# Kernel optimization log

Measured on AMD Instinct MI355X. Metric: run time of the kernel, lower is better.

Reference implementation:

```python
import jax, jax.numpy as jnp
import numpy as np

B, S, T, D, H, HD = 1, 2048, 256, 3072, 24, 128
FF = 4 * D
EPS_LN = 1e-6
EPS_RMS = 1e-6


def _layernorm(x):
    m = jnp.mean(x, axis=-1, keepdims=True)
    v = jnp.mean(jnp.square(x - m), axis=-1, keepdims=True)
    return (x - m) * jax.lax.rsqrt(v + EPS_LN)


def _rmsnorm(x, w):
    return x * jax.lax.rsqrt(jnp.mean(jnp.square(x), axis=-1, keepdims=True) + EPS_RMS) * w


def _rope_interleaved(x, cos, sin):
    # x: [B,S,H,HD], cos/sin: [S,HD//2]; non-neox (interleaved) style
    x1 = x[..., 0::2]
    x2 = x[..., 1::2]
    c = cos[None, :, None, :]
    s = sin[None, :, None, :]
    o1 = x1 * c - x2 * s
    o2 = x2 * c + x1 * s
    return jnp.stack([o1, o2], axis=-1).reshape(x.shape)


def setup_inputs() -> dict:
    key = jax.random.key(0)
    ks = jax.random.split(key, 12)

    def n(k, shape, scale):
        return jax.random.normal(k, shape, dtype=jnp.float32) * scale

    # real RoPE tables
    pos = np.arange(S, dtype=np.float64)
    inv_freq = 1.0 / (10000.0 ** (np.arange(0, HD, 2, dtype=np.float64) / HD))
    ang = np.outer(pos, inv_freq)  # [S, HD//2]

    return {
        "img": n(ks[0], (B, S, D), 1.0),
        "vec": n(ks[1], (B, D), 1.0),
        "cos": jnp.asarray(np.cos(ang), jnp.float32),
        "sin": jnp.asarray(np.sin(ang), jnp.float32),
        "k_txt": n(ks[2], (B, T, H, HD), 1.0),
        "v_txt": n(ks[3], (B, T, H, HD), 1.0),
        "mod_w": n(ks[4], (D, 6 * D), 0.02),
        "mod_b": jnp.zeros((6 * D,), jnp.float32),
        "qkv_w": n(ks[5], (D, 3 * D), 0.02),
        "qkv_b": jnp.zeros((3 * D,), jnp.float32),
        "qn_w": jnp.ones((HD,), jnp.float32),
        "kn_w": jnp.ones((HD,), jnp.float32),
        "proj_w": n(ks[6], (D, D), 0.02),
        "proj_b": jnp.zeros((D,), jnp.float32),
        "mlp_w1": n(ks[7], (D, FF), 0.02),
        "mlp_b1": jnp.zeros((FF,), jnp.float32),
        "mlp_w2": n(ks[8], (FF, D), 0.02),
        "mlp_b2": jnp.zeros((D,), jnp.float32),
    }


def reference(img, vec, cos, sin, k_txt, v_txt, mod_w, mod_b, qkv_w, qkv_b,
              qn_w, kn_w, proj_w, proj_b, mlp_w1, mlp_b1, mlp_w2, mlp_b2):
    # modulation: silu(vec) -> linear -> 6 chunks, each [B,1,D]
    mod = jax.nn.silu(vec) @ mod_w + mod_b
    (a_shift, a_scale, a_gate, m_shift, m_scale, m_gate) = [
        m[:, None, :] for m in jnp.split(mod, 6, axis=-1)
    ]

    # LayerNorm (no affine) + scale/shift modulate
    x = _layernorm(img) * (1.0 + a_scale) + a_shift

    qkv = (x @ qkv_w + qkv_b).reshape(B, S, 3, H, HD)
    q, k, v = qkv[:, :, 0], qkv[:, :, 1], qkv[:, :, 2]
    q = _rmsnorm(q, qn_w)
    k = _rmsnorm(k, kn_w)
    q = _rope_interleaved(q, cos, sin)
    k = _rope_interleaved(k, cos, sin)

    # concat text KV cache (no RoPE on text tokens)
    k_all = jnp.concatenate([k, k_txt], axis=1)  # [B,S+T,H,HD]
    v_all = jnp.concatenate([v, v_txt], axis=1)

    scale = 1.0 / jnp.sqrt(jnp.asarray(HD, jnp.float32))
    scores = jnp.einsum('bqhd,bkhd->bhqk', q, k_all) * scale
    probs = jax.nn.softmax(scores, axis=-1)
    attn = jnp.einsum('bhqk,bkhd->bqhd', probs, v_all).reshape(B, S, D)

    attn_out = attn @ proj_w + proj_b

    # ScaleResidualLayerNormScaleShift
    residual = img + a_gate * attn_out
    mlp_in = _layernorm(residual) * (1.0 + m_scale) + m_shift

    mlp_out = jax.nn.gelu(mlp_in @ mlp_w1 + mlp_b1, approximate=True) @ mlp_w2 + mlp_b2
    return residual + m_gate * mlp_out
```

## Files before the change

### kernel.cpp

```cpp
#include <hip/hip_runtime.h>

typedef short short8 __attribute__((ext_vector_type(8)));
typedef float f32x4 __attribute__((ext_vector_type(4)));

#define DEV static __device__ __forceinline__

DEV unsigned short f2bf(float f) {
  union { float f; unsigned u; } v; v.f = f;
  unsigned u = v.u;
  unsigned r = u + 0x7fffu + ((u >> 16) & 1u);
  return (unsigned short)(r >> 16);
}
DEV float bf2f(unsigned short b) {
  union { unsigned u; float f; } v; v.u = ((unsigned)b) << 16;
  return v.f;
}
DEV void load_lds16(const void* g, void* l) {
  __builtin_amdgcn_global_load_lds(
      (const __attribute__((address_space(1))) unsigned int*)g,
      (__attribute__((address_space(3))) unsigned int*)l, 16, 0, 0);
}
DEV int swz(int L) { return L ^ ((L >> 3) & 0x30); }

__global__ __launch_bounds__(256) void zero_mod(const float* __restrict__ b, float* __restrict__ out) {
  int j = blockIdx.x * 256 + threadIdx.x;
  out[j] = b[j];
}

__global__ __launch_bounds__(256) void mod_gemv(const float* __restrict__ vec,
                                                const float* __restrict__ W,
                                                float* __restrict__ out) {
  __shared__ float sv[192];
  int tid = threadIdx.x;
  int kb = blockIdx.y * 192;
  if (tid < 192) {
    float x = vec[kb + tid];
    sv[tid] = x / (1.f + __expf(-x));
  }
  __syncthreads();
  int j = blockIdx.x * 256 + tid;
  float a0 = 0, a1 = 0, a2 = 0, a3 = 0;
  for (int i = 0; i < 192; i += 4) {
    a0 += sv[i + 0] * W[(size_t)(kb + i + 0) * 18432 + j];
    a1 += sv[i + 1] * W[(size_t)(kb + i + 1) * 18432 + j];
    a2 += sv[i + 2] * W[(size_t)(kb + i + 2) * 18432 + j];
    a3 += sv[i + 3] * W[(size_t)(kb + i + 3) * 18432 + j];
  }
  atomicAdd(&out[j], a0 + a1 + a2 + a3);
}

__global__ __launch_bounds__(256) void ln_kernel(const float* __restrict__ in,
                                                 const float* __restrict__ mod,
                                                 int shift_off, int scale_off,
                                                 unsigned short* __restrict__ out) {
  int rowb = blockIdx.x;
  const float* x = in + (size_t)rowb * 3072;
  int tid = threadIdx.x;
  float s = 0.f, ss = 0.f;
  float4 v[3];
#pragma unroll
  for (int r = 0; r < 3; r++) {
    v[r] = *(const float4*)&x[r * 1024 + tid * 4];
    s += v[r].x + v[r].y + v[r].z + v[r].w;
    ss += v[r].x * v[r].x + v[r].y * v[r].y + v[r].z * v[r].z + v[r].w * v[r].w;
  }
#pragma unroll
  for (int m = 32; m; m >>= 1) { s += __shfl_xor(s, m); ss += __shfl_xor(ss, m); }
  __shared__ float red[8];
  int w = tid >> 6, lane = tid & 63;
  if (lane == 0) { red[w] = s; red[4 + w] = ss; }
  __syncthreads();
  s = red[0] + red[1] + red[2] + red[3];
  ss = red[4] + red[5] + red[6] + red[7];
  float mean = s * (1.f / 3072.f);
  float var = ss * (1.f / 3072.f) - mean * mean;
  float rstd = rsqrtf(var + 1e-6f);
#pragma unroll
  for (int r = 0; r < 3; r++) {
    int c = r * 1024 + tid * 4;
    float xv[4] = {v[r].x, v[r].y, v[r].z, v[r].w};
#pragma unroll
    for (int i = 0; i < 4; i++) {
      float o = (xv[i] - mean) * rstd * (1.f + mod[scale_off + c + i]) + mod[shift_off + c + i];
      out[(size_t)rowb * 3072 + c + i] = f2bf(o);
    }
  }
}

__global__ __launch_bounds__(256) void transpose_k(const float* __restrict__ src,
                                                   unsigned short* __restrict__ dst,
                                                   int K, int N) {
  __shared__ float t[64][65];
  int n0 = blockIdx.x * 64, k0 = blockIdx.y * 64;
  int tid = threadIdx.x;
#pragma unroll
  for (int i = 0; i < 16; i++) {
    int lin = i * 256 + tid;
    int r = lin >> 6, c = lin & 63;
    t[r][c] = src[(size_t)(k0 + r) * N + n0 + c];
  }
  __syncthreads();
#pragma unroll
  for (int i = 0; i < 16; i++) {
    int lin = i * 256 + tid;
    int rn = lin >> 6, cn = lin & 63;
    dst[(size_t)(n0 + rn) * K + k0 + cn] = f2bf(t[cn][rn]);
  }
}

__global__ __launch_bounds__(256) void vt_k(const unsigned short* __restrict__ qkvb,
                                            const float* __restrict__ v_txt,
                                            unsigned short* __restrict__ vt) {
  int h = blockIdx.y;
  int c8 = blockIdx.x * 2 + (threadIdx.x >> 7);
  int d = threadIdx.x & 127;
  int kvb = c8 * 8;
  short8 o;
  if (kvb < 2048) {
#pragma unroll
    for (int j = 0; j < 8; j++)
      o[j] = (short)qkvb[(size_t)(kvb + j) * 9216 + 6144 + h * 128 + d];
  } else {
#pragma unroll
    for (int j = 0; j < 8; j++)
      o[j] = (short)f2bf(v_txt[((size_t)(kvb + j - 2048) * 24 + h) * 128 + d]);
  }
  *(short8*)&vt[((size_t)h * 128 + d) * 2304 + kvb] = o;
}

template <int EPI>
__global__ __launch_bounds__(512, 2) void gemm8(const unsigned short* __restrict__ A,
                                                const unsigned short* __restrict__ Bt,
                                                const float* __restrict__ bias,
                                                unsigned short* __restrict__ outb,
                                                int N, int ldk, int klen, size_t zstride) {
  __shared__ unsigned short As[4][8192];
  __shared__ unsigned short Bs[4][8192];
  const int tid = threadIdx.x, lane = tid & 63, w = tid >> 6;
  const int wr = w >> 2, wc = w & 3;
  const int lr = lane & 15, lk = lane >> 4;

  const int bm = blockIdx.y * 256, bn = blockIdx.x * 256;
  const int kbase = blockIdx.z * klen;
  const int NT = klen >> 5;

  const int D0 = tid * 16;
  const int D1 = 8192 + tid * 16;
  const int L0 = swz(D0), L1 = swz(D1);
  const unsigned short* sA0 = A + (size_t)(bm + (L0 >> 6)) * ldk + kbase + ((L0 & 63) >> 1);
  const unsigned short* sA1 = A + (size_t)(bm + (L1 >> 6)) * ldk + kbase + ((L1 & 63) >> 1);
  const unsigned short* sB0 = Bt + (size_t)(bn + (L0 >> 6)) * ldk + kbase + ((L0 & 63) >> 1);
  const unsigned short* sB1 = Bt + (size_t)(bn + (L1 >> 6)) * ldk + kbase + ((L1 & 63) >> 1);

  int aoff[8], boff[4];
#pragma unroll
  for (int mi = 0; mi < 8; mi++)
    aoff[mi] = swz(((wr * 128 + mi * 16 + lr) << 6) | (lk << 4));
#pragma unroll
  for (int ni = 0; ni < 4; ni++)
    boff[ni] = swz(((wc * 64 + ni * 16 + lr) << 6) | (lk << 4));

  f32x4 acc[8][4];
#pragma unroll
  for (int i = 0; i < 8; i++)
#pragma unroll
    for (int j = 0; j < 4; j++) acc[i][j] = (f32x4){0.f, 0.f, 0.f, 0.f};

#pragma unroll
  for (int j = 0; j < 3; j++) {
    load_lds16(sA0 + j * 32, (char*)As + j * 16384 + D0);
    load_lds16(sA1 + j * 32, (char*)As + j * 16384 + D1);
    load_lds16(sB0 + j * 32, (char*)Bs + j * 16384 + D0);
    load_lds16(sB1 + j * 32, (char*)Bs + j * 16384 + D1);
  }
  asm volatile("s_waitcnt vmcnt(8)" ::: "memory");
  __builtin_amdgcn_sched_barrier(0);
  __builtin_amdgcn_s_barrier();

  for (int t = 0; t < NT; ++t) {
    const int rt = t & 3;
    char* Ab = (char*)As + rt * 16384;
    char* Bb = (char*)Bs + rt * 16384;
    const int ss = (t + 3) & 3;
    const int sk = (t + 3) * 32;
    const bool stg = (t + 3) < NT;

    short8 af[8], bf[4];
#pragma unroll
    for (int mi = 0; mi < 8; mi++) af[mi] = *(const short8*)(Ab + aoff[mi]);
#pragma unroll
    for (int ni = 0; ni < 4; ni++) bf[ni] = *(const short8*)(Bb + boff[ni]);
    if (stg) {
      load_lds16(sA0 + sk, (char*)As + ss * 16384 + D0);
      load_lds16(sA1 + sk, (char*)As + ss * 16384 + D1);
      load_lds16(sB0 + sk, (char*)Bs + ss * 16384 + D0);
      load_lds16(sB1 + sk, (char*)Bs + ss * 16384 + D1);
    }
    __builtin_amdgcn_s_setprio(1);
#pragma unroll
    for (int mi = 0; mi < 8; mi++)
#pragma unroll
      for (int ni = 0; ni < 4; ni++)
        acc[mi][ni] = __builtin_amdgcn_mfma_f32_16x16x32_bf16(af[mi], bf[ni], acc[mi][ni], 0, 0, 0);
    __builtin_amdgcn_s_setprio(0);
    if (t < NT - 3) {
      asm volatile("s_waitcnt vmcnt(8)" ::: "memory");
    } else if (t == NT - 3) {
      asm volatile("s_waitcnt vmcnt(4)" ::: "memory");
    } else if (t == NT - 2) {
      asm volatile("s_waitcnt vmcnt(0)" ::: "memory");
    }
    __builtin_amdgcn_sched_barrier(0);
    __builtin_amdgcn_s_barrier();
  }

  const size_t zoff = (size_t)blockIdx.z * zstride;
#pragma unroll
  for (int mi = 0; mi < 8; mi++) {
#pragma unroll
    for (int ni = 0; ni < 4; ni++) {
      int row0 = bm + wr * 128 + mi * 16 + lk * 4;
      int col = bn + wc * 64 + ni * 16 + lr;
#pragma unroll
      for (int r = 0; r < 4; r++) {
        float vv = acc[mi][ni][r];
        if (EPI == 0) {
          outb[(size_t)(row0 + r) * N + col] = f2bf(vv + bias[col]);
        } else if (EPI == 2) {
          float x = vv + bias[col];
          float y = 0.7978845608028654f * (x + 0.044715f * x * x * x);
          float th = 1.f - 2.f / (__expf(2.f * y) + 1.f);
          outb[(size_t)(row0 + r) * N + col] = f2bf(0.5f * x * (1.f + th));
        } else {
          outb[zoff + (size_t)(row0 + r) * N + col] = f2bf(vv);
        }
      }
    }
  }
}

template <int NS>
__global__ __launch_bounds__(256) void sk_epi(const unsigned short* __restrict__ pb,
                                              const float* __restrict__ bias,
                                              const float* __restrict__ addsrc,
                                              const float* __restrict__ gate,
                                              float* __restrict__ out) {
  const int N = 3072;
  const size_t MN = (size_t)2048 * 3072;
  int row = blockIdx.y;
  int col = blockIdx.x * 1024 + threadIdx.x * 4;
  size_t idx = (size_t)row * N + col;
  float4 a = *(const float4*)(addsrc + idx);
  float4 b = *(const float4*)(bias + col);
  float4 g = *(const float4*)(gate + col);
  float sum[4] = {b.x, b.y, b.z, b.w};
#pragma unroll
  for (int s = 0; s < NS; s++) {
    const unsigned short* p = pb + s * MN + idx;
#pragma unroll
    for (int i = 0; i < 4; i++) sum[i] += bf2f(p[i]);
  }
  float4 o;
  o.x = a.x + g.x * sum[0];
  o.y = a.y + g.y * sum[1];
  o.z = a.z + g.z * sum[2];
  o.w = a.w + g.w * sum[3];
  *(float4*)(out + idx) = o;
}

__global__ __launch_bounds__(256) void sk_epiq(const unsigned short* __restrict__ p0,
                                               const unsigned short* __restrict__ p1,
                                               const float* __restrict__ bias,
                                               unsigned short* __restrict__ out) {
  const int N = 9216;
  int row = blockIdx.y;
  int col = blockIdx.x * 1024 + threadIdx.x * 4;
  size_t idx = (size_t)row * N + col;
#pragma unroll
  for (int i = 0; i < 4; i++)
    out[idx + i] = f2bf(bf2f(p0[idx + i]) + bf2f(p1[idx + i]) + bias[col + i]);
}

__global__ __launch_bounds__(64) void qkv_post(const unsigned short* __restrict__ qkv,
                                               const float* __restrict__ k_txt,
                                               const float* __restrict__ cosb,
                                               const float* __restrict__ sinb,
                                               const float* __restrict__ qn,
                                               const float* __restrict__ kn,
                                               unsigned short* __restrict__ qb,
                                               unsigned short* __restrict__ kb) {
  int s = blockIdx.x, h = blockIdx.y;
  int lane = threadIdx.x;
  int d0 = lane * 2;
  if (s < 2048) {
    const unsigned short* rowp = qkv + (size_t)s * 9216;
    float c = cosb[s * 64 + lane], sn = sinb[s * 64 + lane];
    const float ascale = 0.08838834764831845f;
    {
      float a = bf2f(rowp[h * 128 + d0]), b = bf2f(rowp[h * 128 + d0 + 1]);
      float sq = a * a + b * b;
#pragma unroll
      for (int m = 32; m; m >>= 1) sq += __shfl_xor(sq, m);
      float rr = rsqrtf(sq * (1.f / 128.f) + 1e-6f);
      float x1 = a * rr * qn[d0], x2 = b * rr * qn[d0 + 1];
      float o1 = (x1 * c - x2 * sn) * ascale;
      float o2 = (x2 * c + x1 * sn) * ascale;
      size_t off = ((size_t)h * 2048 + s) * 128 + d0;
      qb[off] = f2bf(o1); qb[off + 1] = f2bf(o2);
    }
    {
      float a = bf2f(rowp[3072 + h * 128 + d0]), b = bf2f(rowp[3072 + h * 128 + d0 + 1]);
      float sq = a * a + b * b;
#pragma unroll
      for (int m = 32; m; m >>= 1) sq += __shfl_xor(sq, m);
      float rr = rsqrtf(sq * (1.f / 128.f) + 1e-6f);
      float x1 = a * rr * kn[d0], x2 = b * rr * kn[d0 + 1];
      float o1 = x1 * c - x2 * sn;
      float o2 = x2 * c + x1 * sn;
      size_t off = ((size_t)h * 2304 + s) * 128 + d0;
      kb[off] = f2bf(o1); kb[off + 1] = f2bf(o2);
    }
  } else {
    int t = s - 2048;
    size_t src = ((size_t)t * 24 + h) * 128 + d0;
    size_t off = ((size_t)h * 2304 + s) * 128 + d0;
    kb[off] = f2bf(k_txt[src]); kb[off + 1] = f2bf(k_txt[src + 1]);
  }
}

__global__ __launch_bounds__(512) void attn_k(const unsigned short* __restrict__ qb,
                                              const unsigned short* __restrict__ kb,
                                              const unsigned short* __restrict__ vt,
                                              unsigned short* __restrict__ out) {
  __shared__ unsigned short Ks[3][8192];
  __shared__ unsigned short Vs[3][8192];
  __shared__ unsigned short Ps[8][32 * 72];
  int h = blockIdx.y, q0 = blockIdx.x * 256;
  int tid = threadIdx.x, lane = tid & 63, w = tid >> 6;
  int lr = lane & 15, lk = lane >> 4;

  const unsigned short* kh = kb + (size_t)h * 2304 * 128;
  const unsigned short* vth = vt + (size_t)h * 128 * 2304;

  short8 qf[2][4];
#pragma unroll
  for (int mi = 0; mi < 2; mi++)
#pragma unroll
    for (int kf = 0; kf < 4; kf++)
      qf[mi][kf] = *(const short8*)&qb[((size_t)h * 2048 + q0 + w * 32 + mi * 16 + lr) * 128 + kf * 32 + lk * 8];

  const int kR0 = (tid * 16) >> 8, kR1 = (tid * 16 + 8192) >> 8;
  const int kCc = ((tid * 16) >> 4) & 15;
  const int kOf0 = kR0 * 128 + ((kCc ^ (kR0 & 15)) * 8);
  const int kOf1 = kR1 * 128 + ((kCc ^ (kR1 & 15)) * 8);
  const int vR0 = (tid * 16) >> 7, vR1 = (tid * 16 + 8192) >> 7;
  const int vCc = ((tid * 16) >> 4) & 7;
  const int vOf0 = vR0 * 2304 + ((vCc ^ (vR0 & 7)) * 8);
  const int vOf1 = vR1 * 2304 + ((vCc ^ (vR1 & 7)) * 8);

  float mrow[2][4], lsum[2][4];
#pragma unroll
  for (int mi = 0; mi < 2; mi++)
#pragma unroll
    for (int r = 0; r < 4; r++) { mrow[mi][r] = -1e30f; lsum[mi][r] = 0.f; }
  f32x4 oacc[2][8];
#pragma unroll
  for (int mi = 0; mi < 2; mi++)
#pragma unroll
    for (int i = 0; i < 8; i++) oacc[mi][i] = (f32x4){0.f, 0.f, 0.f, 0.f};

#pragma unroll
  for (int j = 0; j < 2; j++) {
    int kv = j * 64;
    load_lds16(kh + (size_t)kv * 128 + kOf0, (char*)Ks[j] + tid * 16);
    load_lds16(kh + (size_t)kv * 128 + kOf1, (char*)Ks[j] + tid * 16 + 8192);
    load_lds16(vth + kv + vOf0, (char*)Vs[j] + tid * 16);
    load_lds16(vth + kv + vOf1, (char*)Vs[j] + tid * 16 + 8192);
  }
  asm volatile("s_waitcnt vmcnt(4)" ::: "memory");
  __builtin_amdgcn_sched_barrier(0);
  __builtin_amdgcn_s_barrier();

  int cur = 0, st = 2;
  for (int kt = 0; kt < 36; kt++) {
    if (kt + 2 < 36) {
      int kv2 = (kt + 2) * 64;
      load_lds16(kh + (size_t)kv2 * 128 + kOf0, (char*)Ks[st] + tid * 16);
      load_lds16(kh + (size_t)kv2 * 128 + kOf1, (char*)Ks[st] + tid * 16 + 8192);
      load_lds16(vth + kv2 + vOf0, (char*)Vs[st] + tid * 16);
      load_lds16(vth + kv2 + vOf1, (char*)Vs[st] + tid * 16 + 8192);
    }

    f32x4 sa[2][4];
#pragma unroll
    for (int mi = 0; mi < 2; mi++)
#pragma unroll
      for (int ni = 0; ni < 4; ni++) sa[mi][ni] = (f32x4){0.f, 0.f, 0.f, 0.f};
    __builtin_amdgcn_s_setprio(1);
#pragma unroll
    for (int kf = 0; kf < 4; kf++) {
#pragma unroll
      for (int ni = 0; ni < 4; ni++) {
        int n = ni * 16 + lr;
        short8 bfr = *(const short8*)&Ks[cur][n * 128 + (((kf * 4 + lk) ^ lr) & 15) * 8];
        sa[0][ni] = __builtin_amdgcn_mfma_f32_16x16x32_bf16(qf[0][kf], bfr, sa[0][ni], 0, 0, 0);
        sa[1][ni] = __builtin_amdgcn_mfma_f32_16x16x32_bf16(qf[1][kf], bfr, sa[1][ni], 0, 0, 0);
      }
    }
    __builtin_amdgcn_s_setprio(0);

#pragma unroll
    for (int mi = 0; mi < 2; mi++) {
#pragma unroll
      for (int r = 0; r < 4; r++) {
        float mx = fmaxf(fmaxf(sa[mi][0][r], sa[mi][1][r]), fmaxf(sa[mi][2][r], sa[mi][3][r]));
#pragma unroll
        for (int m = 8; m; m >>= 1) mx = fmaxf(mx, __shfl_xor(mx, m));
        float mold = mrow[mi][r];
        if (mx > mold + 8.f) {
          float alpha = __expf(mold - mx);
          lsum[mi][r] *= alpha;
#pragma unroll
          for (int df = 0; df < 8; df++) oacc[mi][df][r] *= alpha;
          mrow[mi][r] = mx;
          mold = mx;
        }
        float p0 = __expf(sa[mi][0][r] - mold);
        float p1 = __expf(sa[mi][1][r] - mold);
        float p2 = __expf(sa[mi][2][r] - mold);
        float p3 = __expf(sa[mi][3][r] - mold);
        float su = p0 + p1 + p2 + p3;
#pragma unroll
        for (int m = 8; m; m >>= 1) su += __shfl_xor(su, m);
        lsum[mi][r] += su;
        int prow = (mi * 16 + lk * 4 + r) * 72;
        Ps[w][prow + 0 * 16 + lr] = f2bf(p0);
        Ps[w][prow + 1 * 16 + lr] = f2bf(p1);
        Ps[w][prow + 2 * 16 + lr] = f2bf(p2);
        Ps[w][prow + 3 * 16 + lr] = f2bf(p3);
      }
    }

    __builtin_amdgcn_s_setprio(1);
#pragma unroll
    for (int kf2 = 0; kf2 < 2; kf2++) {
      short8 pa0 = *(const short8*)&Ps[w][(0 * 16 + lr) * 72 + kf2 * 32 + lk * 8];
      short8 pa1 = *(const short8*)&Ps[w][(1 * 16 + lr) * 72 + kf2 * 32 + lk * 8];
#pragma unroll
      for (int df = 0; df < 8; df++) {
        int d = df * 16 + lr;
        short8 bv = *(const short8*)&Vs[cur][d * 64 + (((kf2 * 4 + lk) ^ (lr & 7)) & 7) * 8];
        oacc[0][df] = __builtin_amdgcn_mfma_f32_16x16x32_bf16(pa0, bv, oacc[0][df], 0, 0, 0);
        oacc[1][df] = __builtin_amdgcn_mfma_f32_16x16x32_bf16(pa1, bv, oacc[1][df], 0, 0, 0);
      }
    }
    __builtin_amdgcn_s_setprio(0);

    if (kt < 34) {
      asm volatile("s_waitcnt vmcnt(4)" ::: "memory");
    } else if (kt == 34) {
      asm volatile("s_waitcnt vmcnt(0)" ::: "memory");
    }
    __builtin_amdgcn_sched_barrier(0);
    __builtin_amdgcn_s_barrier();
    cur = (cur == 2) ? 0 : cur + 1;
    st = (st == 2) ? 0 : st + 1;
  }

#pragma unroll
  for (int mi = 0; mi < 2; mi++) {
#pragma unroll
    for (int r = 0; r < 4; r++) {
      float inv = 1.f / lsum[mi][r];
      int row = q0 + w * 32 + mi * 16 + lk * 4 + r;
#pragma unroll
      for (int df = 0; df < 8; df++)
        out[(size_t)row * 3072 + h * 128 + df * 16 + lr] = f2bf(oacc[mi][df][r] * inv);
    }
  }
}

extern "C" void kernel_launch(void* const* d_in, const int* in_sizes, int n_in,
                              void* d_out, int out_size, void* d_ws, size_t ws_size,
                              hipStream_t stream) {
  const float* img = (const float*)d_in[0];
  const float* vec = (const float*)d_in[1];
  const float* cosb = (const float*)d_in[2];
  const float* sinb = (const float*)d_in[3];
  const float* k_txt = (const float*)d_in[4];
  const float* v_txt = (const float*)d_in[5];
  const float* mod_w = (const float*)d_in[6];
  const float* mod_b = (const float*)d_in[7];
  const float* qkv_w = (const float*)d_in[8];
  const float* qkv_b = (const float*)d_in[9];
  const float* qn_w = (const float*)d_in[10];
  const float* kn_w = (const float*)d_in[11];
  const float* proj_w = (const float*)d_in[12];
  const float* proj_b = (const float*)d_in[13];
  const float* mlp_w1 = (const float*)d_in[14];
  const float* mlp_b1 = (const float*)d_in[15];
  const float* mlp_w2 = (const float*)d_in[16];
  const float* mlp_b2 = (const float*)d_in[17];
  float* outp = (float*)d_out;

  const size_t MN = (size_t)2048 * 3072;
  char* ws = (char*)d_ws;
  unsigned short* qkvb = (unsigned short*)(ws + 0);
  unsigned short* qbuf = (unsigned short*)(ws + 37748736);
  unsigned short* kbuf = (unsigned short*)(ws + 50331648);
  unsigned short* vtbuf = (unsigned short*)(ws + 64487424);
  unsigned short* attnb = (unsigned short*)(ws + 78643200);
  float* resid = (float*)(ws + 91226112);
  unsigned short* xln = (unsigned short*)(ws + 116391936);
  float* modv = (float*)(ws + 128974848);
  unsigned short* wt = (unsigned short*)(ws + 129048576);
  unsigned short* hbuf = (unsigned short*)(ws + 0);
  unsigned short* qp0 = (unsigned short*)(ws + 37748736);
  unsigned short* qp1 = (unsigned short*)(ws + 78643200);
  const size_t qzstride = (78643200 - 37748736) / 2;
  unsigned short* pbuf = (unsigned short*)(ws + 50331648);

  zero_mod<<<72, 256, 0, stream>>>(mod_b, modv);
  mod_gemv<<<dim3(72, 16), 256, 0, stream>>>(vec, mod_w, modv);

  ln_kernel<<<2048, 256, 0, stream>>>(img, modv, 0, 3072, xln);

  transpose_k<<<dim3(144, 48), 256, 0, stream>>>(qkv_w, wt, 3072, 9216);
  gemm8<3><<<dim3(36, 8, 2), 512, 0, stream>>>(xln, wt, nullptr, qp0, 9216, 3072, 1536, qzstride);
  sk_epiq<<<dim3(9, 2048), 256, 0, stream>>>(qp0, qp1, qkv_b, qkvb);

  qkv_post<<<dim3(2304, 24), 64, 0, stream>>>(qkvb, k_txt, cosb, sinb, qn_w, kn_w, qbuf, kbuf);
  vt_k<<<dim3(144, 24), 256, 0, stream>>>(qkvb, v_txt, vtbuf);

  attn_k<<<dim3(8, 24), 512, 0, stream>>>(qbuf, kbuf, vtbuf, attnb);

  transpose_k<<<dim3(48, 48), 256, 0, stream>>>(proj_w, wt, 3072, 3072);
  gemm8<3><<<dim3(12, 8, 2), 512, 0, stream>>>(attnb, wt, nullptr, pbuf, 3072, 3072, 1536, MN);
  sk_epi<2><<<dim3(3, 2048), 256, 0, stream>>>(pbuf, proj_b, img, modv + 2 * 3072, resid);

  ln_kernel<<<2048, 256, 0, stream>>>(resid, modv, 3 * 3072, 4 * 3072, xln);

  transpose_k<<<dim3(192, 48), 256, 0, stream>>>(mlp_w1, wt, 3072, 12288);
  gemm8<2><<<dim3(48, 8, 1), 512, 0, stream>>>(xln, wt, mlp_b1, hbuf, 12288, 3072, 3072, 0);

  transpose_k<<<dim3(48, 192), 256, 0, stream>>>(mlp_w2, wt, 12288, 3072);
  gemm8<3><<<dim3(12, 8, 2), 512, 0, stream>>>(hbuf, wt, nullptr, pbuf, 3072, 12288, 6144, MN);
  sk_epi<2><<<dim3(3, 2048), 256, 0, stream>>>(pbuf, mlp_b2, resid, modv + 5 * 3072, outp);
}
```

Before: 960.8 us.

## Restructure GEMM main loop into double-buffered 64-wide K tiles with staged quadrant loads

```diff
diff --git a/kernel.cpp b/kernel.cpp
--- a/kernel.cpp
+++ b/kernel.cpp
@@ -134,31 +134,46 @@
                                                 const float* __restrict__ bias,
                                                 unsigned short* __restrict__ outb,
                                                 int N, int ldk, int klen, size_t zstride) {
-  __shared__ unsigned short As[4][8192];
-  __shared__ unsigned short Bs[4][8192];
+  __shared__ unsigned short As[2][16384];
+  __shared__ unsigned short Bs[2][16384];
   const int tid = threadIdx.x, lane = tid & 63, w = tid >> 6;
   const int wr = w >> 2, wc = w & 3;
   const int lr = lane & 15, lk = lane >> 4;
 
   const int bm = blockIdx.y * 256, bn = blockIdx.x * 256;
   const int kbase = blockIdx.z * klen;
-  const int NT = klen >> 5;
-
-  const int D0 = tid * 16;
-  const int D1 = 8192 + tid * 16;
-  const int L0 = swz(D0), L1 = swz(D1);
-  const unsigned short* sA0 = A + (size_t)(bm + (L0 >> 6)) * ldk + kbase + ((L0 & 63) >> 1);
-  const unsigned short* sA1 = A + (size_t)(bm + (L1 >> 6)) * ldk + kbase + ((L1 & 63) >> 1);
-  const unsigned short* sB0 = Bt + (size_t)(bn + (L0 >> 6)) * ldk + kbase + ((L0 & 63) >> 1);
-  const unsigned short* sB1 = Bt + (size_t)(bn + (L1 >> 6)) * ldk + kbase + ((L1 & 63) >> 1);
+  const int NT = klen >> 6;
+
+  const int j0 = tid * 16, j1 = 8192 + tid * 16;
+  const int r0 = j0 >> 7, r1 = j1 >> 7;
+  const int sw0 = ((j0 >> 4) & 7) ^ (r0 & 7);
+  const int sw1 = ((j1 >> 4) & 7) ^ (r1 & 7);
+  const unsigned short* sA0[2] = {A + (size_t)(bm + r0) * ldk + kbase + sw0 * 8,
+                                  A + (size_t)(bm + r1) * ldk + kbase + sw1 * 8};
+  const unsigned short* sA1[2] = {A + (size_t)(bm + 128 + r0) * ldk + kbase + sw0 * 8,
+                                  A + (size_t)(bm + 128 + r1) * ldk + kbase + sw1 * 8};
+  const unsigned short* sB0[2] = {Bt + (size_t)(bn + r0) * ldk + kbase + sw0 * 8,
+                                  Bt + (size_t)(bn + r1) * ldk + kbase + sw1 * 8};
+  const unsigned short* sB1[2] = {Bt + (size_t)(bn + 128 + r0) * ldk + kbase + sw0 * 8,
+                                  Bt + (size_t)(bn + 128 + r1) * ldk + kbase + sw1 * 8};
+
+#define STG(SRC, BASE, HALF, KO)                                          \
+  do {                                                                    \
+    load_lds16(SRC[0] + (KO), (char*)(BASE) + (HALF) * 16384 + j0);       \
+    load_lds16(SRC[1] + (KO), (char*)(BASE) + (HALF) * 16384 + j1);       \
+  } while (0)
 
   int aoff[8], boff[4];
 #pragma unroll
-  for (int mi = 0; mi < 8; mi++)
-    aoff[mi] = swz(((wr * 128 + mi * 16 + lr) << 6) | (lk << 4));
-#pragma unroll
-  for (int ni = 0; ni < 4; ni++)
-    boff[ni] = swz(((wc * 64 + ni * 16 + lr) << 6) | (lk << 4));
+  for (int mi = 0; mi < 8; mi++) {
+    int r = wr * 128 + mi * 16 + lr;
+    aoff[mi] = r * 128 + ((lk ^ (r & 7)) << 4);
+  }
+#pragma unroll
+  for (int ni = 0; ni < 4; ni++) {
+    int r = wc * 64 + ni * 16 + lr;
+    boff[ni] = r * 128 + ((lk ^ (r & 7)) << 4);
+  }
 
   f32x4 acc[8][4];
 #pragma unroll
@@ -166,53 +181,107 @@
 #pragma unroll
     for (int j = 0; j < 4; j++) acc[i][j] = (f32x4){0.f, 0.f, 0.f, 0.f};
 
-#pragma unroll
-  for (int j = 0; j < 3; j++) {
-    load_lds16(sA0 + j * 32, (char*)As + j * 16384 + D0);
-    load_lds16(sA1 + j * 32, (char*)As + j * 16384 + D1);
-    load_lds16(sB0 + j * 32, (char*)Bs + j * 16384 + D0);
-    load_lds16(sB1 + j * 32, (char*)Bs + j * 16384 + D1);
-  }
-  asm volatile("s_waitcnt vmcnt(8)" ::: "memory");
+  STG(sA0, As[0], 0, 0);
+  STG(sA1, As[0], 1, 0);
+  STG(sB0, Bs[0], 0, 0);
+  STG(sB1, Bs[0], 1, 0);
+  if (1 < NT) STG(sA0, As[1], 0, 64);
+  asm volatile("s_waitcnt vmcnt(2)" ::: "memory");
   __builtin_amdgcn_sched_barrier(0);
   __builtin_amdgcn_s_barrier();
 
   for (int t = 0; t < NT; ++t) {
-    const int rt = t & 3;
-    char* Ab = (char*)As + rt * 16384;
-    char* Bb = (char*)Bs + rt * 16384;
-    const int ss = (t + 3) & 3;
-    const int sk = (t + 3) * 32;
-    const bool stg = (t + 3) < NT;
-
-    short8 af[8], bf[4];
-#pragma unroll
-    for (int mi = 0; mi < 8; mi++) af[mi] = *(const short8*)(Ab + aoff[mi]);
-#pragma unroll
-    for (int ni = 0; ni < 4; ni++) bf[ni] = *(const short8*)(Bb + boff[ni]);
-    if (stg) {
-      load_lds16(sA0 + sk, (char*)As + ss * 16384 + D0);
-      load_lds16(sA1 + sk, (char*)As + ss * 16384 + D1);
-      load_lds16(sB0 + sk, (char*)Bs + ss * 16384 + D0);
-      load_lds16(sB1 + sk, (char*)Bs + ss * 16384 + D1);
-    }
+    const int cb = t & 1, nb = cb ^ 1;
+    char* Ab = (char*)As + cb * 32768;
+    char* Bb = (char*)Bs + cb * 32768;
+    const int k1 = (t + 1) * 64, k2 = (t + 2) * 64;
+
+    short8 aq[4][2], bq[4][2];
+#pragma unroll
+    for (int mi = 0; mi < 4; mi++) {
+      aq[mi][0] = *(const short8*)(Ab + aoff[mi]);
+      aq[mi][1] = *(const short8*)(Ab + (aoff[mi] ^ 64));
+    }
+#pragma unroll
+    for (int ni = 0; ni < 2; ni++) {
+      bq[ni][0] = *(const short8*)(Bb + boff[ni]);
+      bq[ni][1] = *(const short8*)(Bb + (boff[ni] ^ 64));
+    }
+    if (t + 1 < NT) STG(sA1, As[nb], 1, k1);
+    __builtin_amdgcn_s_barrier();
+    asm volatile("s_waitcnt lgkmcnt(0)" ::: "memory");
+    __builtin_amdgcn_sched_barrier(0);
     __builtin_amdgcn_s_setprio(1);
 #pragma unroll
-    for (int mi = 0; mi < 8; mi++)
-#pragma unroll
-      for (int ni = 0; ni < 4; ni++)
-        acc[mi][ni] = __builtin_amdgcn_mfma_f32_16x16x32_bf16(af[mi], bf[ni], acc[mi][ni], 0, 0, 0);
+    for (int mi = 0; mi < 4; mi++)
+#pragma unroll
+      for (int ni = 0; ni < 2; ni++)
+#pragma unroll
+        for (int kk = 0; kk < 2; kk++)
+          acc[mi][ni] = __builtin_amdgcn_mfma_f32_16x16x32_bf16(aq[mi][kk], bq[ni][kk], acc[mi][ni], 0, 0, 0);
     __builtin_amdgcn_s_setprio(0);
-    if (t < NT - 3) {
-      asm volatile("s_waitcnt vmcnt(8)" ::: "memory");
-    } else if (t == NT - 3) {
-      asm volatile("s_waitcnt vmcnt(4)" ::: "memory");
+    __builtin_amdgcn_s_barrier();
+
+#pragma unroll
+    for (int ni = 2; ni < 4; ni++) {
+      bq[ni][0] = *(const short8*)(Bb + boff[ni]);
+      bq[ni][1] = *(const short8*)(Bb + (boff[ni] ^ 64));
+    }
+    if (t + 1 < NT) STG(sB0, Bs[nb], 0, k1);
+    __builtin_amdgcn_s_barrier();
+    asm volatile("s_waitcnt lgkmcnt(0)" ::: "memory");
+    __builtin_amdgcn_sched_barrier(0);
+    __builtin_amdgcn_s_setprio(1);
+#pragma unroll
+    for (int mi = 0; mi < 4; mi++)
+#pragma unroll
+      for (int ni = 2; ni < 4; ni++)
+#pragma unroll
+        for (int kk = 0; kk < 2; kk++)
+          acc[mi][ni] = __builtin_amdgcn_mfma_f32_16x16x32_bf16(aq[mi][kk], bq[ni][kk], acc[mi][ni], 0, 0, 0);
+    __builtin_amdgcn_s_setprio(0);
+    __builtin_amdgcn_s_barrier();
+
+#pragma unroll
+    for (int mi = 0; mi < 4; mi++) {
+      aq[mi][0] = *(const short8*)(Ab + aoff[mi + 4]);
+      aq[mi][1] = *(const short8*)(Ab + (aoff[mi + 4] ^ 64));
+    }
+    if (t + 1 < NT) STG(sB1, Bs[nb], 1, k1);
+    __builtin_amdgcn_s_barrier();
+    asm volatile("s_waitcnt lgkmcnt(0)" ::: "memory");
+    __builtin_amdgcn_sched_barrier(0);
+    __builtin_amdgcn_s_setprio(1);
+#pragma unroll
+    for (int mi = 0; mi < 4; mi++)
+#pragma unroll
+      for (int ni = 0; ni < 2; ni++)
+#pragma unroll
+        for (int kk = 0; kk < 2; kk++)
+          acc[mi + 4][ni] = __builtin_amdgcn_mfma_f32_16x16x32_bf16(aq[mi][kk], bq[ni][kk], acc[mi + 4][ni], 0, 0, 0);
+    __builtin_amdgcn_s_setprio(0);
+    __builtin_amdgcn_s_barrier();
+
+    if (t + 2 < NT) STG(sA0, As[cb], 0, k2);
+    __builtin_amdgcn_s_barrier();
+    __builtin_amdgcn_s_setprio(1);
+#pragma unroll
+    for (int mi = 0; mi < 4; mi++)
+#pragma unroll
+      for (int ni = 2; ni < 4; ni++)
+#pragma unroll
+        for (int kk = 0; kk < 2; kk++)
+          acc[mi + 4][ni] = __builtin_amdgcn_mfma_f32_16x16x32_bf16(aq[mi][kk], bq[ni][kk], acc[mi + 4][ni], 0, 0, 0);
+    __builtin_amdgcn_s_setprio(0);
+    if (t < NT - 2) {
+      asm volatile("s_waitcnt vmcnt(2)" ::: "memory");
     } else if (t == NT - 2) {
       asm volatile("s_waitcnt vmcnt(0)" ::: "memory");
     }
     __builtin_amdgcn_sched_barrier(0);
     __builtin_amdgcn_s_barrier();
   }
+#undef STG
 
   const size_t zoff = (size_t)blockIdx.z * zstride;
 #pragma unroll
```

Result: slower. 981.1 us (+2.1%).
